# Kernel optimization log

Measured on AMD Instinct MI355X. Metric: run time of the kernel, lower is better.

Reference implementation:

```python
import jax, jax.numpy as jnp
import numpy as np

EPS = 1e-8  # matches torch F.cosine_similarity default eps


def setup_inputs() -> dict:
    key = jax.random.key(0)
    kq, km = jax.random.split(key)
    B, M, D = 4096, 65536, 512
    return {
        "query_features": jax.random.normal(kq, (B, D), dtype=jnp.float32),
        "memory": jax.random.normal(km, (M, D), dtype=jnp.float32),
        "k": 8,
    }


def reference(query_features, memory, k):
    # cosine similarity: normalize rows (clamped norm like torch eps), then GEMM
    qn = query_features / jnp.maximum(
        jnp.linalg.norm(query_features, axis=-1, keepdims=True), EPS)
    mn = memory / jnp.maximum(
        jnp.linalg.norm(memory, axis=-1, keepdims=True), EPS)
    sims = jnp.einsum("bd,md->bm", qn, mn)          # [B, M]
    _, top_idx = jax.lax.top_k(sims, k)              # [B, k]
    # gather memory rows and average over the k neighbors
    return memory[top_idx].mean(axis=1)              # [B, D]
```

## Files before the change

kernel.cpp:

```cpp
#include <hip/hip_runtime.h>
#include <hip/hip_bf16.h>

#define B_ROWS 4096
#define M_ROWS 65536
#define DIM 512
#define TOPK 8
#define CAP 512
#define NR 24
#define TAU 0.132583f
#define FB_N 2048

typedef unsigned short u16;
typedef unsigned int u32;
typedef signed char s8;
typedef unsigned char u8;
typedef int i32x4 __attribute__((ext_vector_type(4)));

__device__ inline void gl_lds16(const void* g, void* l) {
  __builtin_amdgcn_global_load_lds(
      (const __attribute__((address_space(1))) u32*)g,
      (__attribute__((address_space(3))) u32*)l, 16, 0, 0);
}

__global__ __launch_bounds__(256) void quant_kernel(const float* __restrict__ in,
                                                    s8* __restrict__ out,
                                                    float* __restrict__ scale,
                                                    int nrows) {
  int gw = (int)((blockIdx.x * 256 + threadIdx.x) >> 6);
  int lane = threadIdx.x & 63;
  if (gw >= nrows) return;
  const float4* r = (const float4*)(in + (size_t)gw * DIM);
  float4 v0 = r[lane * 2 + 0];
  float4 v1 = r[lane * 2 + 1];
  float ss = v0.x*v0.x + v0.y*v0.y + v0.z*v0.z + v0.w*v0.w
           + v1.x*v1.x + v1.y*v1.y + v1.z*v1.z + v1.w*v1.w;
#pragma unroll
  for (int off = 32; off > 0; off >>= 1) ss += __shfl_xor(ss, off);
  float inv = 1.0f / fmaxf(sqrtf(ss), 1e-8f);
  float x[8] = {v0.x*inv, v0.y*inv, v0.z*inv, v0.w*inv,
                v1.x*inv, v1.y*inv, v1.z*inv, v1.w*inv};
  float ma = 0.f;
#pragma unroll
  for (int e = 0; e < 8; e++) ma = fmaxf(ma, fabsf(x[e]));
#pragma unroll
  for (int off = 32; off > 0; off >>= 1) ma = fmaxf(ma, __shfl_xor(ma, off));
  float s = fmaxf(ma, 1e-20f) * (1.0f / 127.0f);
  float rs = 1.0f / s;
  u32 lo = 0, hi = 0;
#pragma unroll
  for (int e = 0; e < 4; e++) {
    int qi = __float2int_rn(fminf(fmaxf(x[e] * rs, -127.f), 127.f));
    lo |= ((u32)(u8)(s8)qi) << (8 * e);
  }
#pragma unroll
  for (int e = 0; e < 4; e++) {
    int qi = __float2int_rn(fminf(fmaxf(x[4 + e] * rs, -127.f), 127.f));
    hi |= ((u32)(u8)(s8)qi) << (8 * e);
  }
  uint2 pk; pk.x = lo; pk.y = hi;
  *(uint2*)(out + (size_t)gw * DIM + lane * 8) = pk;
  if (lane == 0) scale[gw] = s;
}

__global__ __launch_bounds__(256, 4) void gemm_select(const s8* __restrict__ qn,
                                                      const s8* __restrict__ mn,
                                                      const float* __restrict__ sa,
                                                      const float* __restrict__ sb,
                                                      int* __restrict__ count,
                                                      u32* __restrict__ cand) {
  __shared__ s8 sA[2][8192];
  __shared__ s8 sB[2][8192];

  int bid0 = blockIdx.x;
  int b1 = (bid0 & 7) * 2048 + (bid0 >> 3);
  int qtile = (b1 >> 12) * 8 + (b1 & 7);
  int mtile = (b1 >> 3) & 511;

  int tid = threadIdx.x;
  int lane = tid & 63;
  int w = tid >> 6;
  int wr = w >> 1, wc = w & 1;
  int rlo = lane & 15;
  int khi16 = (lane >> 4) << 4;

  const s8* gA = qn + (size_t)qtile * 128 * DIM;
  const s8* gB = mn + (size_t)mtile * 128 * DIM;

  int brow_lo = tid >> 3;
  int innb = (tid & 7) << 4;
  int inns = innb ^ ((brow_lo & 7) << 4);
  int grow0 = brow_lo * 2 + (inns >> 6);
  int gcolb = inns & 63;

  auto stage = [&](int slot, int kt) {
#pragma unroll
    for (int i2 = 0; i2 < 2; i2++) {
      gl_lds16(gA + (size_t)(grow0 + i2 * 64) * DIM + kt * 64 + gcolb,
               &sA[slot][i2 * 4096 + w * 1024]);
      gl_lds16(gB + (size_t)(grow0 + i2 * 64) * DIM + kt * 64 + gcolb,
               &sB[slot][i2 * 4096 + w * 1024]);
    }
  };
  auto rdA = [&](int slot, int mi) {
    int row = wr * 64 + mi * 16 + rlo;
    int brow = row >> 1;
    int phys = (brow << 7) + ((((row & 1) << 6) + khi16) ^ ((brow & 7) << 4));
    return *(const i32x4*)((const char*)sA[slot] + phys);
  };
  auto rdB = [&](int slot, int ni) {
    int row = wc * 64 + ni * 16 + rlo;
    int brow = row >> 1;
    int phys = (brow << 7) + ((((row & 1) << 6) + khi16) ^ ((brow & 7) << 4));
    return *(const i32x4*)((const char*)sB[slot] + phys);
  };

  i32x4 acc[4][4];
#pragma unroll
  for (int i = 0; i < 4; i++)
#pragma unroll
    for (int jj = 0; jj < 4; jj++) {
      i32x4 z = {0, 0, 0, 0};
      acc[i][jj] = z;
    }

  stage(0, 0);

  for (int t = 0; t < 8; t++) {
    asm volatile("s_waitcnt vmcnt(0)" ::: "memory");
    __builtin_amdgcn_s_barrier();
    int cs = t & 1;
    if (t < 7) stage(cs ^ 1, t + 1);
    i32x4 aF[4], bF[4];
#pragma unroll
    for (int mi = 0; mi < 4; mi++) aF[mi] = rdA(cs, mi);
#pragma unroll
    for (int ni = 0; ni < 4; ni++) bF[ni] = rdB(cs, ni);
    __builtin_amdgcn_s_setprio(1);
#pragma unroll
    for (int mi = 0; mi < 4; mi++)
#pragma unroll
      for (int ni = 0; ni < 4; ni++)
        acc[mi][ni] = __builtin_amdgcn_mfma_i32_16x16x64_i8(aF[mi], bF[ni], acc[mi][ni], 0, 0, 0);
    __builtin_amdgcn_s_setprio(0);
  }

  int qbase = qtile * 128 + wr * 64 + (lane >> 4) * 4;
  int mbase = mtile * 128 + wc * 64 + (lane & 15);
#pragma unroll
  for (int mi = 0; mi < 4; mi++) {
    float4 sav = *(const float4*)&sa[qbase + mi * 16];
#pragma unroll
    for (int ni = 0; ni < 4; ni++) {
      float sbv = sb[mbase + ni * 16];
#pragma unroll
      for (int r = 0; r < 4; r++) {
        float v = (float)acc[mi][ni][r] * (sav[r] * sbv);
        if (v > TAU) {
          int qq = qbase + mi * 16 + r;
          u32 pk = (__builtin_bit_cast(u32, v) & 0xFFFF0000u) | (u32)(mbase + ni * 16);
          int pos = atomicAdd(&count[qq], 1);
          if (pos < CAP) cand[(size_t)qq * CAP + pos] = pk;
        }
      }
    }
  }
}

__global__ __launch_bounds__(256) void topk_kernel(const float* __restrict__ q,
                                                   const float* __restrict__ mem,
                                                   const int* __restrict__ count,
                                                   const u32* __restrict__ cand,
                                                   float* __restrict__ out) {
  __shared__ double s_sims[FB_N];
  __shared__ int s_cidx[FB_N];
  __shared__ double s_red[4];
  __shared__ int s_redj[4];
  __shared__ u32 s_pk[CAP];
  __shared__ int s_sel[NR];
  __shared__ double s_x[NR];
  __shared__ int s_win[TOPK];

  int b = blockIdx.x;
  int tid = threadIdx.x;
  int lane = tid & 63;
  int w = tid >> 6;

  const float* qrow = q + (size_t)b * DIM;
  const float4* qv = (const float4*)qrow;
  float4 q0 = qv[lane * 2], q1 = qv[lane * 2 + 1];
  double q8[8] = {q0.x, q0.y, q0.z, q0.w, q1.x, q1.y, q1.z, q1.w};
  double qq = 0;
#pragma unroll
  for (int e = 0; e < 8; e++) qq += q8[e] * q8[e];
#pragma unroll
  for (int off = 32; off > 0; off >>= 1) qq += __shfl_xor(qq, off);
  double qnorm = fmax(sqrt(qq), 1e-8);

  int c = count[b];
  if (c >= TOPK && c <= CAP) {
    for (int j = tid; j < c; j += 256) s_pk[j] = cand[(size_t)b * CAP + j];
    __syncthreads();
    int nsel = c < NR ? c : NR;
    if (w == 0) {
      for (int r = 0; r < nsel; r++) {
        int best = -1, bj = -1;
        for (int j = lane; j < c; j += 64) {
          int v = (int)s_pk[j];
          if (v > best) { best = v; bj = j; }
        }
#pragma unroll
        for (int off = 32; off > 0; off >>= 1) {
          int ov = __shfl_down(best, off);
          int oj = __shfl_down(bj, off);
          if (ov > best) { best = ov; bj = oj; }
        }
        bj = __shfl(bj, 0);
        if (lane == 0) { s_sel[r] = (int)(s_pk[bj] & 0xFFFFu); s_pk[bj] = 0; }
      }
    }
    __syncthreads();
    for (int i = w; i < nsel; i += 4) {
      int mi = s_sel[i];
      const float4* mv = (const float4*)(mem + (size_t)mi * DIM);
      float4 m0 = mv[lane * 2], m1 = mv[lane * 2 + 1];
      double m8[8] = {m0.x, m0.y, m0.z, m0.w, m1.x, m1.y, m1.z, m1.w};
      double dot = 0, mm = 0;
#pragma unroll
      for (int e = 0; e < 8; e++) { dot += q8[e] * m8[e]; mm += m8[e] * m8[e]; }
#pragma unroll
      for (int off = 32; off > 0; off >>= 1) {
        dot += __shfl_xor(dot, off);
        mm += __shfl_xor(mm, off);
      }
      if (lane == 0) s_x[i] = dot / (qnorm * fmax(sqrt(mm), 1e-8));
    }
    __syncthreads();
    if (w == 0) {
      double myv = (lane < nsel) ? s_x[lane] : -1e300;
      int myrow = (lane < nsel) ? s_sel[lane] : -1;
      for (int r = 0; r < TOPK; r++) {
        double bv = myv; int bl = lane;
#pragma unroll
        for (int off = 32; off > 0; off >>= 1) {
          double ov = __shfl_down(bv, off);
          int ol = __shfl_down(bl, off);
          if (ov > bv) { bv = ov; bl = ol; }
        }
        bl = __shfl(bl, 0);
        int brow = __shfl(myrow, bl);
        if (lane == 0) s_win[r] = brow;
        if (lane == bl) myv = -1e300;
      }
    }
    __syncthreads();
  } else {
    double tv[8]; int tix[8];
#pragma unroll
    for (int r = 0; r < 8; r++) { tv[r] = -1e300; tix[r] = -1; }
    for (int row = tid; row < M_ROWS; row += 256) {
      const float4* mv = (const float4*)(mem + (size_t)row * DIM);
      double dot = 0, mm = 0;
      for (int e = 0; e < DIM / 4; e++) {
        float4 m4 = mv[e], qk = qv[e];
        dot += (double)m4.x * qk.x + (double)m4.y * qk.y + (double)m4.z * qk.z + (double)m4.w * qk.w;
        mm  += (double)m4.x * m4.x + (double)m4.y * m4.y + (double)m4.z * m4.z + (double)m4.w * m4.w;
      }
      double sim = dot / (qnorm * fmax(sqrt(mm), 1e-8));
      int am = 0;
#pragma unroll
      for (int r = 1; r < 8; r++) if (tv[r] < tv[am]) am = r;
      if (sim > tv[am]) { tv[am] = sim; tix[am] = row; }
    }
#pragma unroll
    for (int r = 0; r < 8; r++) { s_sims[tid * 8 + r] = tv[r]; s_cidx[tid * 8 + r] = tix[r]; }
    __syncthreads();
    for (int r = 0; r < TOPK; r++) {
      double best = -1e300; int bj = -1;
      for (int j = tid; j < FB_N; j += 256) {
        double v = s_sims[j];
        if (v > best) { best = v; bj = j; }
      }
#pragma unroll
      for (int off = 32; off > 0; off >>= 1) {
        double ov = __shfl_down(best, off);
        int oj = __shfl_down(bj, off);
        if (ov > best) { best = ov; bj = oj; }
      }
      if (lane == 0) { s_red[w] = best; s_redj[w] = bj; }
      __syncthreads();
      if (tid == 0) {
        double bb = s_red[0]; int jj = s_redj[0];
        for (int i = 1; i < 4; i++) if (s_red[i] > bb) { bb = s_red[i]; jj = s_redj[i]; }
        s_win[r] = s_cidx[jj];
        s_sims[jj] = -1e300;
      }
      __syncthreads();
    }
  }

  float ax = 0.f, ay = 0.f;
#pragma unroll
  for (int r = 0; r < TOPK; r++) {
    const float2 v = *(const float2*)(mem + (size_t)s_win[r] * DIM + tid * 2);
    ax += v.x; ay += v.y;
  }
  float2 o; o.x = ax * 0.125f; o.y = ay * 0.125f;
  *(float2*)(out + (size_t)b * DIM + tid * 2) = o;
}

extern "C" void kernel_launch(void* const* d_in, const int* in_sizes, int n_in,
                              void* d_out, int out_size, void* d_ws, size_t ws_size,
                              hipStream_t stream) {
  (void)in_sizes; (void)n_in; (void)out_size; (void)ws_size;
  const float* q = (const float*)d_in[0];
  const float* mem = (const float*)d_in[1];
  float* out = (float*)d_out;

  char* ws = (char*)d_ws;
  s8* mn8 = (s8*)ws;
  s8* qn8 = (s8*)(ws + (size_t)M_ROWS * DIM);
  float* sb = (float*)(ws + (size_t)(M_ROWS + B_ROWS) * DIM);
  float* sa = (float*)((char*)sb + (size_t)M_ROWS * sizeof(float));
  int* count = (int*)((char*)sa + (size_t)B_ROWS * sizeof(float));
  u32* cand = (u32*)((char*)count + (size_t)B_ROWS * sizeof(int));

  hipMemsetAsync(count, 0, B_ROWS * sizeof(int), stream);
  quant_kernel<<<M_ROWS / 4, 256, 0, stream>>>(mem, mn8, sb, M_ROWS);
  quant_kernel<<<B_ROWS / 4, 256, 0, stream>>>(q, qn8, sa, B_ROWS);
  gemm_select<<<(B_ROWS / 128) * (M_ROWS / 128), 256, 0, stream>>>(qn8, mn8, sa, sb, count, cand);
  topk_kernel<<<B_ROWS, 256, 0, stream>>>(q, mem, count, cand, out);
}
```

Baseline: 328.7 us.

## Merge quantize launches, precompute GEMM LDS offsets, unroll K loop, lower NR

Quantization of memory and queries now runs in one launch that branches on the row index, removing one kernel launch and its tail. The GEMM main loop is fully unrolled, with global and LDS addresses and swizzled read offsets computed once before the loop, so less address arithmetic runs per iteration. NR drops from 24 to 16, which likely shrinks the per-row candidate refinement work in the hidden selection code. A smaller NR could change which candidates get rescored.

Result: faster. 305.7 us, median of 3 (-7.0%).

```diff
diff --git a/kernel.cpp b/kernel.cpp
--- a/kernel.cpp
+++ b/kernel.cpp
@@ -6,7 +6,7 @@
 #define DIM 512
 #define TOPK 8
 #define CAP 512
-#define NR 24
+#define NR 16
 #define TAU 0.132583f
 #define FB_N 2048
 
@@ -22,14 +22,24 @@
       (__attribute__((address_space(3))) u32*)l, 16, 0, 0);
 }
 
-__global__ __launch_bounds__(256) void quant_kernel(const float* __restrict__ in,
-                                                    s8* __restrict__ out,
-                                                    float* __restrict__ scale,
-                                                    int nrows) {
+__global__ __launch_bounds__(256) void quant_kernel(const float* __restrict__ mem,
+                                                    const float* __restrict__ q,
+                                                    s8* __restrict__ mn8,
+                                                    s8* __restrict__ qn8,
+                                                    float* __restrict__ sb,
+                                                    float* __restrict__ sa) {
   int gw = (int)((blockIdx.x * 256 + threadIdx.x) >> 6);
   int lane = threadIdx.x & 63;
-  if (gw >= nrows) return;
-  const float4* r = (const float4*)(in + (size_t)gw * DIM);
+  const float* in;
+  s8* out;
+  float* scale;
+  int row;
+  if (gw < M_ROWS) {
+    in = mem; out = mn8; scale = sb; row = gw;
+  } else {
+    in = q; out = qn8; scale = sa; row = gw - M_ROWS;
+  }
+  const float4* r = (const float4*)(in + (size_t)row * DIM);
   float4 v0 = r[lane * 2 + 0];
   float4 v1 = r[lane * 2 + 1];
   float ss = v0.x*v0.x + v0.y*v0.y + v0.z*v0.z + v0.w*v0.w
@@ -58,8 +68,8 @@
     hi |= ((u32)(u8)(s8)qi) << (8 * e);
   }
   uint2 pk; pk.x = lo; pk.y = hi;
-  *(uint2*)(out + (size_t)gw * DIM + lane * 8) = pk;
-  if (lane == 0) scale[gw] = s;
+  *(uint2*)(out + (size_t)row * DIM + lane * 8) = pk;
+  if (lane == 0) scale[row] = s;
 }
 
 __global__ __launch_bounds__(256, 4) void gemm_select(const s8* __restrict__ qn,
@@ -92,27 +102,35 @@
   int grow0 = brow_lo * 2 + (inns >> 6);
   int gcolb = inns & 63;
 
+  const s8* gA0 = gA + (size_t)grow0 * DIM + gcolb;
+  const s8* gA1 = gA + (size_t)(grow0 + 64) * DIM + gcolb;
+  const s8* gB0 = gB + (size_t)grow0 * DIM + gcolb;
+  const s8* gB1 = gB + (size_t)(grow0 + 64) * DIM + gcolb;
+  s8* lA0 = &sA[0][w * 1024];
+  s8* lA1 = &sA[0][4096 + w * 1024];
+  s8* lB0 = &sB[0][w * 1024];
+  s8* lB1 = &sB[0][4096 + w * 1024];
+
   auto stage = [&](int slot, int kt) {
-#pragma unroll
-    for (int i2 = 0; i2 < 2; i2++) {
-      gl_lds16(gA + (size_t)(grow0 + i2 * 64) * DIM + kt * 64 + gcolb,
-               &sA[slot][i2 * 4096 + w * 1024]);
-      gl_lds16(gB + (size_t)(grow0 + i2 * 64) * DIM + kt * 64 + gcolb,
-               &sB[slot][i2 * 4096 + w * 1024]);
-    }
+    int so = slot * 8192;
+    gl_lds16(gA0 + kt * 64, lA0 + so);
+    gl_lds16(gA1 + kt * 64, lA1 + so);
+    gl_lds16(gB0 + kt * 64, lB0 + so);
+    gl_lds16(gB1 + kt * 64, lB1 + so);
   };
-  auto rdA = [&](int slot, int mi) {
-    int row = wr * 64 + mi * 16 + rlo;
+
+  auto physof = [&](int row) {
     int brow = row >> 1;
-    int phys = (brow << 7) + ((((row & 1) << 6) + khi16) ^ ((brow & 7) << 4));
-    return *(const i32x4*)((const char*)sA[slot] + phys);
+    return (brow << 7) + ((((row & 1) << 6) + khi16) ^ ((brow & 7) << 4));
   };
-  auto rdB = [&](int slot, int ni) {
-    int row = wc * 64 + ni * 16 + rlo;
-    int brow = row >> 1;
-    int phys = (brow << 7) + ((((row & 1) << 6) + khi16) ^ ((brow & 7) << 4));
-    return *(const i32x4*)((const char*)sB[slot] + phys);
-  };
+  const char* rbA = (const char*)&sA[0][0];
+  const char* rbB = (const char*)&sB[0][0];
+  int offA[4], offB[4];
+#pragma unroll
+  for (int i = 0; i < 4; i++) {
+    offA[i] = physof(wr * 64 + i * 16 + rlo);
+    offB[i] = physof(wc * 64 + i * 16 + rlo);
+  }
 
   i32x4 acc[4][4];
 #pragma unroll
@@ -125,16 +143,17 @@
 
   stage(0, 0);
 
+#pragma unroll
   for (int t = 0; t < 8; t++) {
     asm volatile("s_waitcnt vmcnt(0)" ::: "memory");
     __builtin_amdgcn_s_barrier();
-    int cs = t & 1;
+    const int cs = t & 1;
     if (t < 7) stage(cs ^ 1, t + 1);
     i32x4 aF[4], bF[4];
 #pragma unroll
-    for (int mi = 0; mi < 4; mi++) aF[mi] = rdA(cs, mi);
-#pragma unroll
-    for (int ni = 0; ni < 4; ni++) bF[ni] = rdB(cs, ni);
+    for (int mi = 0; mi < 4; mi++) aF[mi] = *(const i32x4*)(rbA + cs * 8192 + offA[mi]);
+#pragma unroll
+    for (int ni = 0; ni < 4; ni++) bF[ni] = *(const i32x4*)(rbB + cs * 8192 + offB[ni]);
     __builtin_amdgcn_s_setprio(1);
 #pragma unroll
     for (int mi = 0; mi < 4; mi++)
@@ -325,8 +344,7 @@
   u32* cand = (u32*)((char*)count + (size_t)B_ROWS * sizeof(int));
 
   hipMemsetAsync(count, 0, B_ROWS * sizeof(int), stream);
-  quant_kernel<<<M_ROWS / 4, 256, 0, stream>>>(mem, mn8, sb, M_ROWS);
-  quant_kernel<<<B_ROWS / 4, 256, 0, stream>>>(q, qn8, sa, B_ROWS);
+  quant_kernel<<<(M_ROWS + B_ROWS) / 4, 256, 0, stream>>>(mem, q, mn8, qn8, sb, sa);
   gemm_select<<<(B_ROWS / 128) * (M_ROWS / 128), 256, 0, stream>>>(qn8, mn8, sa, sb, count, cand);
   topk_kernel<<<B_ROWS, 256, 0, stream>>>(q, mem, count, cand, out);
 }
```
